# Kernel tuning notes

Measured on AMD Instinct MI355X. Metric: run time of the kernel, lower is better.

## Reference

```python
import jax, jax.numpy as jnp
import numpy as np

N = 32000      # total nodes (16 graphs x 2000 nodes)
B = 16         # batch of graphs
NPG = N // B   # nodes per graph
K = 1600       # assign_dim (total clusters)
KPG = K // B   # clusters per graph
D = 128        # input_dim == output_feat_dim
E = 512000     # edges (avg degree 16), block-diagonal across graphs


def setup_inputs() -> dict:
    key = jax.random.key(0)
    ks = jax.random.split(key, 12)
    # block-structured edge list: each edge stays within its graph
    epg = E // B
    gid = jnp.repeat(jnp.arange(B, dtype=jnp.int32), epg) * NPG
    src = gid + jax.random.randint(ks[0], (E,), 0, NPG, dtype=jnp.int32)
    dst = gid + jax.random.randint(ks[1], (E,), 0, NPG, dtype=jnp.int32)
    h = jax.random.normal(ks[2], (N, D), dtype=jnp.float32)
    s = 0.05
    return {
        'h': h, 'src': src, 'dst': dst,
        'W1f': jax.random.normal(ks[3], (D, D), jnp.float32) * s,
        'b1f': jnp.zeros((D,), jnp.float32),
        'W2f': jax.random.normal(ks[4], (D, D), jnp.float32) * s,
        'b2f': jnp.zeros((D,), jnp.float32),
        'W1p': jax.random.normal(ks[5], (D, K), jnp.float32) * s,
        'b1p': jnp.zeros((K,), jnp.float32),
        'W2p': jax.random.normal(ks[6], (K, K), jnp.float32) * s,
        'b2p': jnp.zeros((K,), jnp.float32),
    }


def _gin(h, src, dst, W1, b1, W2, b2):
    # mean-aggregate neighbor features, then 2-layer MLP (histocartography GINLayer)
    deg = jax.ops.segment_sum(jnp.ones((src.shape[0],), h.dtype), dst, num_segments=N)
    agg = jax.ops.segment_sum(h[src], dst, num_segments=N)
    agg = agg / jnp.maximum(deg, 1.0)[:, None]
    x = h + agg
    x = jax.nn.relu(x @ W1 + b1)
    x = jax.nn.relu(x @ W2 + b2)
    return x


def _forward(h, src, dst, W1f, b1f, W2f, b2f, W1p, b1p, W2p, b2p):
    feat = _gin(h, src, dst, W1f, b1f, W2f, b2f)            # [N, D]
    assign = _gin(h, src, dst, W1p, b1p, W2p, b2p)          # [N, K]
    # block-diagonal mask: node of graph b can only assign to clusters of graph b
    node_gid = jnp.arange(N, dtype=jnp.int32) // NPG
    col_gid = jnp.arange(K, dtype=jnp.int32) // KPG
    mask = (node_gid[:, None] == col_gid[None, :]).astype(assign.dtype)  # [N, K]
    # masked_softmax(memory_efficient=False): softmax(x*mask)*mask, renormalized
    p = jax.nn.softmax(assign * mask, axis=-1) * mask
    assign = p / (jnp.sum(p, axis=-1, keepdims=True) + 1e-13)
    h_pool = assign.T @ feat                                # [K, D]
    # adj @ assign where adj[dst, src] = 1 (sparse-dense mm via scatter)
    tmp = jax.ops.segment_sum(assign[src], dst, num_segments=N)  # [N, K]
    adj_new = assign.T @ tmp                                # [K, K]
    return adj_new, h_pool


def reference(h, src, dst, W1f, b1f, W2f, b2f, W1p, b1p, W2p, b2p):
    return _forward(h, src, dst, W1f, b1f, W2f, b2f, W1p, b1p, W2p, b2p)
```

## Files before the change

kernel.cpp:

```cpp
#include <hip/hip_runtime.h>

#define N_NODES 32000
#define NPG     2000
#define NGRAPH  16
#define K_ASSIGN 1600
#define KPG     100
#define D_FEAT  128
#define N_EDGES 512000

typedef float f32x4 __attribute__((ext_vector_type(4)));
typedef __bf16 bf16x8 __attribute__((ext_vector_type(8)));

union FragU { unsigned u[4]; bf16x8 v; };

__device__ __forceinline__ float frelu(float v) { return fmaxf(v, 0.0f); }

__device__ __forceinline__ unsigned short f2bf(float f) {
  unsigned u = __float_as_uint(f);
  u += 0x7FFFu + ((u >> 16) & 1u);
  return (unsigned short)(u >> 16);
}
__device__ __forceinline__ float bfLO(unsigned v) { return __uint_as_float(v << 16); }
__device__ __forceinline__ float bfHI(unsigned v) { return __uint_as_float(v & 0xFFFF0000u); }

__global__ __launch_bounds__(256) void scan_counts(
    const int* __restrict__ cnt, int* __restrict__ rowstart) {
  __shared__ int sums[256];
  int t = threadIdx.x;
  int base = t * 125;
  int s = 0;
  for (int i = 0; i < 125; i++) s += cnt[base + i];
  sums[t] = s;
  __syncthreads();
  for (int off = 1; off < 256; off <<= 1) {
    int v = (t >= off) ? sums[t - off] : 0;
    __syncthreads();
    sums[t] += v;
    __syncthreads();
  }
  int run = (t == 0) ? 0 : sums[t - 1];
  for (int i = 0; i < 125; i++) {
    rowstart[base + i] = run;
    run += cnt[base + i];
  }
  if (t == 255) rowstart[32000] = run;
}

__global__ __launch_bounds__(256) void edge_fill(
    const int* __restrict__ src, const int* __restrict__ dst,
    const int* __restrict__ rowstart, int* __restrict__ cursor,
    int* __restrict__ bucket) {
  int e = blockIdx.x * 256 + threadIdx.x;
  if (e < N_EDGES) {
    int d = dst[e];
    int pos = atomicAdd(&cursor[d], 1);
    bucket[rowstart[d] + pos] = src[e];
  }
}

__global__ __launch_bounds__(256) void prep_all(
    const float* __restrict__ W1f, const float* __restrict__ W2f,
    const float* __restrict__ W1p, const float* __restrict__ W2p,
    unsigned short* __restrict__ o1, unsigned short* __restrict__ o2,
    unsigned short* __restrict__ o3, unsigned short* __restrict__ o4,
    const float* __restrict__ h, unsigned short* __restrict__ h_bf,
    const int* __restrict__ dst, int* __restrict__ cnt) {
  __shared__ float tile[32][33];
  int b = blockIdx.x;
  int t = threadIdx.x;
  if (b >= 6732) {
    int e = (b - 6732) * 256 + t;
    if (e < N_EDGES) atomicAdd(&cnt[dst[e]], 1);
    return;
  }
  if (b >= 2732) {
    int i = (b - 2732) * 256 + t;
    float4 v = ((const float4*)h)[i];
    ushort4 o;
    o.x = f2bf(v.x); o.y = f2bf(v.y); o.z = f2bf(v.z); o.w = f2bf(v.w);
    ((ushort4*)h_bf)[i] = o;
    return;
  }
  const float* in;
  unsigned short* out;
  int R, C, rb;
  if (b < 16)       { in = W1f; out = o1; R = 128;  C = 128;  rb = b; }
  else if (b < 32)  { in = W2f; out = o2; R = 128;  C = 128;  rb = b - 16; }
  else if (b < 232) { in = W1p; out = o3; R = 128;  C = 1600; rb = b - 32; }
  else              { in = W2p; out = o4; R = 1600; C = 1600; rb = b - 232; }
  int ct = C >> 5;
  int bc = rb % ct, br = rb / ct;
  int r0 = br * 32, c0 = bc * 32;
#pragma unroll
  for (int i = 0; i < 4; i++) {
    int r = (t >> 5) + i * 8, c = t & 31;
    tile[r][c] = in[(size_t)(r0 + r) * C + c0 + c];
  }
  __syncthreads();
#pragma unroll
  for (int i = 0; i < 4; i++) {
    int c = (t >> 5) + i * 8, r = t & 31;
    out[(size_t)(c0 + c) * R + r0 + r] = f2bf(tile[r][c]);
  }
}

__global__ __launch_bounds__(256) void gin_gather(
    const int* __restrict__ rowstart, const int* __restrict__ bucket,
    const unsigned short* __restrict__ h_bf, unsigned short* __restrict__ x_bf) {
  int bid = (int)(blockIdx.x & 7) * 1000 + (int)(blockIdx.x >> 3);
  int n = bid * 4 + (threadIdx.x >> 6);
  int lane = threadIdx.x & 63;
  int rs = rowstart[n], re = rowstart[n + 1];
  const unsigned* hb = (const unsigned*)h_bf;
  float ax = 0.f, ay = 0.f;
  int e = rs;
  for (; e + 4 <= re; e += 4) {
    unsigned v0 = hb[(size_t)bucket[e] * 64 + lane];
    unsigned v1 = hb[(size_t)bucket[e + 1] * 64 + lane];
    unsigned v2 = hb[(size_t)bucket[e + 2] * 64 + lane];
    unsigned v3 = hb[(size_t)bucket[e + 3] * 64 + lane];
    ax += (bfLO(v0) + bfLO(v1)) + (bfLO(v2) + bfLO(v3));
    ay += (bfHI(v0) + bfHI(v1)) + (bfHI(v2) + bfHI(v3));
  }
  for (; e < re; e++) {
    unsigned v = hb[(size_t)bucket[e] * 64 + lane];
    ax += bfLO(v);
    ay += bfHI(v);
  }
  float invd = 1.0f / fmaxf((float)(re - rs), 1.0f);
  unsigned hv = hb[(size_t)n * 64 + lane];
  unsigned o = ((unsigned)f2bf(bfHI(hv) + ay * invd) << 16) |
               f2bf(bfLO(hv) + ax * invd);
  ((unsigned*)x_bf)[(size_t)n * 64 + lane] = o;
}

#define FF_STR 136
__global__ __launch_bounds__(512) void feat_fused(
    const unsigned short* __restrict__ x_bf,
    const unsigned short* __restrict__ w1t, const float* __restrict__ b1f,
    const unsigned short* __restrict__ w2t, const float* __restrict__ b2f,
    unsigned short* __restrict__ feat_bf) {
  __shared__ __align__(16) unsigned char smem[2 * 34816];
  unsigned short* xa = (unsigned short*)smem;
  unsigned short* ws = (unsigned short*)(smem + 34816);
  int t = threadIdx.x;
  size_t base = (size_t)blockIdx.x * 128;

#pragma unroll
  for (int i = 0; i < 4; i++) {
    int fi = t + 512 * i;
    int r = fi >> 4, u8 = (fi & 15) * 8;
    *(uint4*)&xa[r * FF_STR + u8] = *(const uint4*)(x_bf + (base + r) * 128 + u8);
    *(uint4*)&ws[r * FF_STR + u8] = *(const uint4*)(w1t + (size_t)r * 128 + u8);
  }
  __syncthreads();

  int w = t >> 6, l = t & 63, lr = l & 15, lg = l >> 4;
  int myrow = 16 * w + lr;
  bf16x8 af[4];
#pragma unroll
  for (int kc = 0; kc < 4; kc++)
    af[kc] = *(bf16x8*)&xa[myrow * FF_STR + 32 * kc + 8 * lg];

  f32x4 p[8];
#pragma unroll
  for (int ntk = 0; ntk < 8; ntk++) {
    p[ntk] = (f32x4){0.f, 0.f, 0.f, 0.f};
    int c = 16 * ntk + lr;
#pragma unroll
    for (int kc = 0; kc < 4; kc++) {
      bf16x8 wf = *(bf16x8*)&ws[c * FF_STR + 32 * kc + 8 * lg];
      p[ntk] = __builtin_amdgcn_mfma_f32_16x16x32_bf16(wf, af[kc], p[ntk], 0, 0, 0);
    }
  }
  __syncthreads();

#pragma unroll
  for (int ntk = 0; ntk < 8; ntk++) {
    int kk0 = 16 * ntk + 4 * lg;
    float4 b1 = *(const float4*)(b1f + kk0);
    ushort4 pk;
    pk.x = f2bf(frelu(p[ntk][0] + b1.x));
    pk.y = f2bf(frelu(p[ntk][1] + b1.y));
    pk.z = f2bf(frelu(p[ntk][2] + b1.z));
    pk.w = f2bf(frelu(p[ntk][3] + b1.w));
    *(ushort4*)&xa[myrow * FF_STR + kk0] = pk;
  }
#pragma unroll
  for (int i = 0; i < 4; i++) {
    int fi = t + 512 * i;
    int r = fi >> 4, u8 = (fi & 15) * 8;
    *(uint4*)&ws[r * FF_STR + u8] = *(const uint4*)(w2t + (size_t)r * 128 + u8);
  }
  __syncthreads();

  bf16x8 a2[4];
#pragma unroll
  for (int kc = 0; kc < 4; kc++)
    a2[kc] = *(bf16x8*)&xa[myrow * FF_STR + 32 * kc + 8 * lg];
#pragma unroll
  for (int nt = 0; nt < 8; nt++) {
    f32x4 q = (f32x4){0.f, 0.f, 0.f, 0.f};
    int c = 16 * nt + lr;
#pragma unroll
    for (int kc = 0; kc < 4; kc++) {
      bf16x8 wf = *(bf16x8*)&ws[c * FF_STR + 32 * kc + 8 * lg];
      q = __builtin_amdgcn_mfma_f32_16x16x32_bf16(wf, a2[kc], q, 0, 0, 0);
    }
    int c0 = 16 * nt + 4 * lg;
    float4 b2 = *(const float4*)(b2f + c0);
    ushort4 pk;
    pk.x = f2bf(frelu(q[0] + b2.x));
    pk.y = f2bf(frelu(q[1] + b2.y));
    pk.z = f2bf(frelu(q[2] + b2.z));
    pk.w = f2bf(frelu(q[3] + b2.w));
    *(ushort4*)&feat_bf[(base + myrow) * 128 + c0] = pk;
  }
}

#define FA_WS 136
#define FA_PS 72
#define FA_W1OFF 17408
#define FA_W2BASE 34816
#define FA_W2OFF 16128
__global__ __launch_bounds__(512) void fused_assign_sm(
    const unsigned short* __restrict__ x_bf, const unsigned short* __restrict__ w1t,
    const float* __restrict__ b1p, const unsigned short* __restrict__ w2t,
    const float* __restrict__ b2p, unsigned short* __restrict__ assign_bf) {
  __shared__ __align__(16) unsigned char smem[67072];
  unsigned short* xt = (unsigned short*)smem;

  int t = threadIdx.x;
  int g = blockIdx.x >> 4;
  int row0 = (blockIdx.x & 15) << 7;
  int n0 = g * NPG + row0;

#pragma unroll
  for (int i = 0; i < 4; i++) {
    int fi = t + 512 * i;
    int r = fi >> 4, u8 = (fi & 15) * 8;
    uint4 v = make_uint4(0, 0, 0, 0);
    if (row0 + r < NPG) v = *(const uint4*)(x_bf + (size_t)(n0 + r) * 128 + u8);
    *(uint4*)&xt[r * FA_WS + u8] = v;
  }
  __syncthreads();

  int w = t >> 6, l = t & 63, lr = l & 15, lg = l >> 4;
  int rh = w >> 1, h = w & 1;

  bf16x8 af[2][4];
#pragma unroll
  for (int ct = 0; ct < 2; ct++)
#pragma unroll
    for (int kc = 0; kc < 4; kc++)
      af[ct][kc] =
          *(bf16x8*)&xt[(32 * rh + 16 * ct + lr) * FA_WS + 32 * kc + 8 * lg];
  __syncthreads();

  {
    unsigned short* w1s = (unsigned short*)smem;
    unsigned short* w2s = (unsigned short*)(smem + FA_W2BASE);
#pragma unroll
    for (int i = 0; i < 2; i++) {
      int fi = t + 512 * i;
      int c = fi >> 4, u8 = (fi & 15) * 8;
      *(uint4*)&w1s[c * FA_WS + u8] = *(const uint4*)(w1t + (size_t)c * 128 + u8);
    }
#pragma unroll
    for (int i = 0; i < 2; i++) {
      int fi = t + 512 * i;
      if (fi < 896) {
        int c = fi >> 3, u8 = (fi & 7) * 8;
        uint4 v = make_uint4(0, 0, 0, 0);
        if (c < KPG)
          v = *(const uint4*)(w2t + (size_t)(g * KPG + c) * K_ASSIGN + u8);
        *(uint4*)&w2s[c * FA_PS + u8] = v;
      }
    }
  }
  __syncthreads();

  f32x4 acc[7][2];
#pragma unroll
  for (int i = 0; i < 7; i++) {
    acc[i][0] = (f32x4){0.f, 0.f, 0.f, 0.f};
    acc[i][1] = (f32x4){0.f, 0.f, 0.f, 0.f};
  }

  for (int cch = 0; cch < 25; cch++) {
    int cur = cch & 1;
    int k0 = cch * 64;
    const unsigned short* w1c = (const unsigned short*)(smem + cur * FA_W1OFF);
    const unsigned short* w2c =
        (const unsigned short*)(smem + FA_W2BASE + cur * FA_W2OFF);
    bool pf = (cch < 24);
    uint4 rA[2], rB[2];
    if (pf) {
      int k1 = k0 + 64;
#pragma unroll
      for (int i = 0; i < 2; i++) {
        int fi = t + 512 * i;
        int c = fi >> 4, u8 = (fi & 15) * 8;
        rA[i] = *(const uint4*)(w1t + (size_t)(k1 + c) * 128 + u8);
      }
#pragma unroll
      for (int i = 0; i < 2; i++) {
        int fi = t + 512 * i;
        rB[i] = make_uint4(0, 0, 0, 0);
        if (fi < 896) {
          int c = fi >> 3, u8 = (fi & 7) * 8;
          if (c < KPG)
            rB[i] = *(const uint4*)(w2t + (size_t)(g * KPG + c) * K_ASSIGN +
                                    k1 + u8);
        }
      }
    }

    f32x4 p[2][2];
    __builtin_amdgcn_s_setprio(1);
#pragma unroll
    for (int nt2 = 0; nt2 < 2; nt2++) {
      p[nt2][0] = (f32x4){0.f, 0.f, 0.f, 0.f};
      p[nt2][1] = (f32x4){0.f, 0.f, 0.f, 0.f};
      int nt = 2 * h + nt2;
#pragma unroll
      for (int kc = 0; kc < 4; kc++) {
        bf16x8 wf = *(bf16x8*)&w1c[(16 * nt + lr) * FA_WS + 32 * kc + 8 * lg];
        p[nt2][0] = __builtin_amdgcn_mfma_f32_16x16x32_bf16(wf, af[0][kc],
                                                            p[nt2][0], 0, 0, 0);
        p[nt2][1] = __builtin_amdgcn_mfma_f32_16x16x32_bf16(wf, af[1][kc],
                                                            p[nt2][1], 0, 0, 0);
      }
    }
    __builtin_amdgcn_s_setprio(0);
    unsigned q[2][2][2];
#pragma unroll
    for (int nt2 = 0; nt2 < 2; nt2++) {
      int kkb = k0 + 16 * (2 * h + nt2) + 4 * lg;
      float4 b1 = *(const float4*)(b1p + kkb);
#pragma unroll
      for (int ct = 0; ct < 2; ct++) {
        float r0 = frelu(p[nt2][ct][0] + b1.x);
        float r1 = frelu(p[nt2][ct][1] + b1.y);
        float r2 = frelu(p[nt2][ct][2] + b1.z);
        float r3 = frelu(p[nt2][ct][3] + b1.w);
        q[nt2][ct][0] = ((unsigned)f2bf(r1) << 16) | f2bf(r0);
        q[nt2][ct][1] = ((unsigned)f2bf(r3) << 16) | f2bf(r2);
      }
    }
    int sA = lr + 32 * (lg & 1);
    int sB = sA + 16;
    bool hi = (lg >= 2);
    FragU pa[2];
#pragma unroll
    for (int ct = 0; ct < 2; ct++) {
      unsigned a0 = (unsigned)__shfl((int)q[0][ct][0], sA, 64);
      unsigned b0 = (unsigned)__shfl((int)q[1][ct][0], sA, 64);
      unsigned a1 = (unsigned)__shfl((int)q[0][ct][1], sA, 64);
      unsigned b1u = (unsigned)__shfl((int)q[1][ct][1], sA, 64);
      unsigned a2 = (unsigned)__shfl((int)q[0][ct][0], sB, 64);
      unsigned b2u = (unsigned)__shfl((int)q[1][ct][0], sB, 64);
      unsigned a3 = (unsigned)__shfl((int)q[0][ct][1], sB, 64);
      unsigned b3u = (unsigned)__shfl((int)q[1][ct][1], sB, 64);
      pa[ct].u[0] = hi ? b0 : a0;
      pa[ct].u[1] = hi ? b1u : a1;
      pa[ct].u[2] = hi ? b2u : a2;
      pa[ct].u[3] = hi ? b3u : a3;
    }
    __builtin_amdgcn_s_setprio(1);
#pragma unroll
    for (int ct2 = 0; ct2 < 7; ct2++) {
      bf16x8 wv = *(bf16x8*)&w2c[(16 * ct2 + lr) * FA_PS + 32 * h + 8 * lg];
      acc[ct2][0] = __builtin_amdgcn_mfma_f32_16x16x32_bf16(wv, pa[0].v,
                                                            acc[ct2][0], 0, 0, 0);
      acc[ct2][1] = __builtin_amdgcn_mfma_f32_16x16x32_bf16(wv, pa[1].v,
                                                            acc[ct2][1], 0, 0, 0);
    }
    __builtin_amdgcn_s_setprio(0);
    if (pf) {
      unsigned short* w1n = (unsigned short*)(smem + (cur ^ 1) * FA_W1OFF);
      unsigned short* w2n =
          (unsigned short*)(smem + FA_W2BASE + (cur ^ 1) * FA_W2OFF);
#pragma unroll
      for (int i = 0; i < 2; i++) {
        int fi = t + 512 * i;
        int c = fi >> 4, u8 = (fi & 15) * 8;
        *(uint4*)&w1n[c * FA_WS + u8] = rA[i];
      }
#pragma unroll
      for (int i = 0; i < 2; i++) {
        int fi = t + 512 * i;
        if (fi < 896) {
          int c = fi >> 3, u8 = (fi & 7) * 8;
          *(uint4*)&w2n[c * FA_PS + u8] = rB[i];
        }
      }
    }
    __syncthreads();
  }

  float* red = (float*)smem;
  if (h == 1) {
#pragma unroll
    for (int ct2 = 0; ct2 < 7; ct2++)
#pragma unroll
      for (int ct = 0; ct < 2; ct++)
        *(f32x4*)&red[((rh * 14 + ct2 * 2 + ct) * 64 + l) * 4] = acc[ct2][ct];
  }
  __syncthreads();
  if (h == 0) {
#pragma unroll
    for (int ct2 = 0; ct2 < 7; ct2++)
#pragma unroll
      for (int ct = 0; ct < 2; ct++)
        acc[ct2][ct] += *(f32x4*)&red[((rh * 14 + ct2 * 2 + ct) * 64 + l) * 4];

#pragma unroll
    for (int ct = 0; ct < 2; ct++) {
      int xrow = row0 + 32 * rh + 16 * ct + lr;
      float v[7][4];
      float m = 0.0f;
#pragma unroll
      for (int ct2 = 0; ct2 < 7; ct2++) {
        int col0 = 16 * ct2 + 4 * lg;
        if (col0 < KPG) {
          float4 b2 = *(const float4*)(b2p + g * KPG + col0);
          v[ct2][0] = frelu(acc[ct2][ct][0] + b2.x);
          v[ct2][1] = frelu(acc[ct2][ct][1] + b2.y);
          v[ct2][2] = frelu(acc[ct2][ct][2] + b2.z);
          v[ct2][3] = frelu(acc[ct2][ct][3] + b2.w);
          m = fmaxf(m, fmaxf(fmaxf(v[ct2][0], v[ct2][1]),
                             fmaxf(v[ct2][2], v[ct2][3])));
        }
      }
      m = fmaxf(m, __shfl_xor(m, 16, 64));
      m = fmaxf(m, __shfl_xor(m, 32, 64));
      float s = 0.0f;
#pragma unroll
      for (int ct2 = 0; ct2 < 7; ct2++) {
        int col0 = 16 * ct2 + 4 * lg;
        if (col0 < KPG) {
          v[ct2][0] = expf(v[ct2][0] - m);
          v[ct2][1] = expf(v[ct2][1] - m);
          v[ct2][2] = expf(v[ct2][2] - m);
          v[ct2][3] = expf(v[ct2][3] - m);
          s += (v[ct2][0] + v[ct2][1]) + (v[ct2][2] + v[ct2][3]);
        }
      }
      s += __shfl_xor(s, 16, 64);
      s += __shfl_xor(s, 32, 64);
      float denom = s + (float)(K_ASSIGN - KPG) * expf(-m);
      float scale = 1.0f / (s + 1e-13f * denom);
      if (xrow < NPG) {
#pragma unroll
        for (int ct2 = 0; ct2 < 7; ct2++) {
          int col0 = 16 * ct2 + 4 * lg;
          if (col0 < KPG) {
            ushort4 pk;
            pk.x = f2bf(v[ct2][0] * scale);
            pk.y = f2bf(v[ct2][1] * scale);
            pk.z = f2bf(v[ct2][2] * scale);
            pk.w = f2bf(v[ct2][3] * scale);
            *(ushort4*)(assign_bf + ((size_t)g * NPG + xrow) * KPG + col0) = pk;
          }
        }
      }
    }
  }
}

__global__ __launch_bounds__(256) void tmp_gather(
    const int* __restrict__ rowstart, const int* __restrict__ bucket,
    const unsigned short* __restrict__ assign_bf, unsigned short* __restrict__ tmp_bf) {
  int bid = (int)(blockIdx.x & 7) * 1000 + (int)(blockIdx.x >> 3);
  int n = bid * 4 + (threadIdx.x >> 6);
  int lane = threadIdx.x & 63;
  if (lane >= 50) return;
  int rs = rowstart[n], re = rowstart[n + 1];
  const unsigned* ab = (const unsigned*)assign_bf;
  float ax = 0.f, ay = 0.f;
  int e = rs;
  for (; e + 4 <= re; e += 4) {
    unsigned v0 = ab[(size_t)bucket[e] * 50 + lane];
    unsigned v1 = ab[(size_t)bucket[e + 1] * 50 + lane];
    unsigned v2 = ab[(size_t)bucket[e + 2] * 50 + lane];
    unsigned v3 = ab[(size_t)bucket[e + 3] * 50 + lane];
    ax += (bfLO(v0) + bfLO(v1)) + (bfLO(v2) + bfLO(v3));
    ay += (bfHI(v0) + bfHI(v1)) + (bfHI(v2) + bfHI(v3));
  }
  for (; e < re; e++) {
    unsigned v = ab[(size_t)bucket[e] * 50 + lane];
    ax += bfLO(v);
    ay += bfHI(v);
  }
  unsigned o = ((unsigned)f2bf(ay) << 16) | f2bf(ax);
  ((unsigned*)tmp_bf)[(size_t)n * 50 + lane] = o;
}

#define PA_STR 72
#define PA_CH 16
#define PA_CHN 128
__global__ __launch_bounds__(256) void pool_adj_mfma(
    const unsigned short* __restrict__ assign_bf,
    const unsigned short* __restrict__ feat_bf,
    const unsigned short* __restrict__ tmp_bf,
    float* __restrict__ out_adj, float* __restrict__ out_hpool) {
  __shared__ __align__(16) unsigned short as[112 * PA_STR];
  __shared__ __align__(16) unsigned short bs[128 * PA_STR];
  bool is_pool = blockIdx.x < NGRAPH * PA_CH;
  int bb = is_pool ? blockIdx.x : blockIdx.x - NGRAPH * PA_CH;
  int g = bb >> 4, ch = bb & 15;
  int nbase = ch * PA_CHN;
  int lim = NPG - nbase;
  if (lim > PA_CHN) lim = PA_CHN;
  int t = threadIdx.x;
  int w = t >> 6, l = t & 63, lr = l & 15, lg = l >> 4;
  const unsigned* au = (const unsigned*)assign_bf;
  const unsigned* fu = (const unsigned*)feat_bf;
  const unsigned* tu = (const unsigned*)tmp_bf;

  for (int i = t; i < 12 * PA_STR; i += 256) as[100 * PA_STR + i] = 0;
  for (int i = t; i < 28 * PA_STR; i += 256) bs[100 * PA_STR + i] = 0;

  f32x4 acc[7][2];
#pragma unroll
  for (int i = 0; i < 7; i++) {
    acc[i][0] = (f32x4){0.f, 0.f, 0.f, 0.f};
    acc[i][1] = (f32x4){0.f, 0.f, 0.f, 0.f};
  }

  for (int kt = 0; kt < 2; kt++) {
    int nt0 = kt * 64;
    __syncthreads();
#pragma unroll
    for (int i = 0; i < 13; i++) {
      int idx = t + 256 * i;
      if (idx < 3200) {
        int r = idx / 50, cu = idx % 50;
        int nl = nt0 + r;
        unsigned v = 0;
        if (nl < lim) v = au[(size_t)(g * NPG + nbase + nl) * 50 + cu];
        as[(2 * cu) * PA_STR + r] = (unsigned short)(v & 0xFFFFu);
        as[(2 * cu + 1) * PA_STR + r] = (unsigned short)(v >> 16);
      }
    }
    if (is_pool) {
#pragma unroll
      for (int i = 0; i < 16; i++) {
        int idx = t + 256 * i;
        int r = idx >> 6, cu = idx & 63;
        int nl = nt0 + r;
        unsigned v = 0;
        if (nl < lim) v = fu[(size_t)(g * NPG + nbase + nl) * 64 + cu];
        bs[(2 * cu) * PA_STR + r] = (unsigned short)(v & 0xFFFFu);
        bs[(2 * cu + 1) * PA_STR + r] = (unsigned short)(v >> 16);
      }
    } else {
#pragma unroll
      for (int i = 0; i < 13; i++) {
        int idx = t + 256 * i;
        if (idx < 3200) {
          int r = idx / 50, cu = idx % 50;
          int nl = nt0 + r;
          unsigned v = 0;
          if (nl < lim) v = tu[(size_t)(g * NPG + nbase + nl) * 50 + cu];
          bs[(2 * cu) * PA_STR + r] = (unsigned short)(v & 0xFFFFu);
          bs[(2 * cu + 1) * PA_STR + r] = (unsigned short)(v >> 16);
        }
      }
    }
    __syncthreads();
#pragma unroll
    for (int kc = 0; kc < 2; kc++) {
      bf16x8 afr[7];
#pragma unroll
      for (int mt = 0; mt < 7; mt++)
        afr[mt] = *(bf16x8*)&as[(16 * mt + lr) * PA_STR + 32 * kc + 8 * lg];
#pragma unroll
      for (int nt2 = 0; nt2 < 2; nt2++) {
        int nt = 2 * w + nt2;
        bf16x8 bfr = *(bf16x8*)&bs[(16 * nt + lr) * PA_STR + 32 * kc + 8 * lg];
#pragma unroll
        for (int mt = 0; mt < 7; mt++)
          acc[mt][nt2] =
              __builtin_amdgcn_mfma_f32_16x16x32_bf16(afr[mt], bfr, acc[mt][nt2], 0, 0, 0);
      }
    }
  }

  if (is_pool) {
#pragma unroll
    for (int mt = 0; mt < 7; mt++)
#pragma unroll
      for (int nt2 = 0; nt2 < 2; nt2++) {
        int nt = 2 * w + nt2;
#pragma unroll
        for (int r = 0; r < 4; r++) {
          int m = 16 * mt + 4 * lg + r;
          if (m < KPG)
            atomicAdd(out_hpool + ((size_t)g * KPG + m) * 128 + 16 * nt + lr,
                      acc[mt][nt2][r]);
        }
      }
  } else {
#pragma unroll
    for (int mt = 0; mt < 7; mt++)
#pragma unroll
      for (int nt2 = 0; nt2 < 2; nt2++) {
        int nt = 2 * w + nt2;
        if (nt < 7) {
          int k2 = 16 * nt + lr;
          if (k2 < KPG) {
#pragma unroll
            for (int r = 0; r < 4; r++) {
              int m = 16 * mt + 4 * lg + r;
              if (m < KPG)
                atomicAdd(out_adj + ((size_t)g * KPG + m) * K_ASSIGN + g * KPG + k2,
                          acc[mt][nt2][r]);
            }
          }
        }
      }
  }
}

extern "C" void kernel_launch(void* const* d_in, const int* in_sizes, int n_in,
                              void* d_out, int out_size, void* d_ws,
                              size_t ws_size, hipStream_t stream) {
  (void)in_sizes; (void)n_in; (void)ws_size;
  const float* h   = (const float*)d_in[0];
  const int*   src = (const int*)d_in[1];
  const int*   dst = (const int*)d_in[2];
  const float* W1f = (const float*)d_in[3];
  const float* b1f = (const float*)d_in[4];
  const float* W2f = (const float*)d_in[5];
  const float* b2f = (const float*)d_in[6];
  const float* W1p = (const float*)d_in[7];
  const float* b1p = (const float*)d_in[8];
  const float* W2p = (const float*)d_in[9];
  const float* b2p = (const float*)d_in[10];

  float* out_adj   = (float*)d_out;
  float* out_hpool = out_adj + (size_t)K_ASSIGN * K_ASSIGN;

  char* ws = (char*)d_ws;
  int* deg_cnt  = (int*)(ws + 0);
  int* rowstart = (int*)(ws + 128000);
  int* cursor   = (int*)(ws + 256032);
  int* bucket   = (int*)(ws + 384032);
  unsigned short* h_bf      = (unsigned short*)(ws + 2432032);
  unsigned short* x_bf      = (unsigned short*)(ws + 10624032);
  unsigned short* feat_bf   = (unsigned short*)(ws + 18816032);
  unsigned short* assign_bf = (unsigned short*)(ws + 27008032);
  unsigned short* tmp_bf    = (unsigned short*)(ws + 33408032);
  unsigned short* w1f_t     = (unsigned short*)(ws + 39808032);
  unsigned short* w2f_t     = (unsigned short*)(ws + 39840800);
  unsigned short* w1p_t     = (unsigned short*)(ws + 39873568);
  unsigned short* w2p_t     = (unsigned short*)(ws + 40283168);

  hipMemsetAsync(deg_cnt, 0, 128000, stream);
  hipMemsetAsync(cursor, 0, 128000, stream);
  hipMemsetAsync(d_out, 0, (size_t)out_size * sizeof(float), stream);

  prep_all<<<8732, 256, 0, stream>>>(W1f, W2f, W1p, W2p, w1f_t, w2f_t, w1p_t,
                                     w2p_t, h, h_bf, dst, deg_cnt);

  scan_counts<<<1, 256, 0, stream>>>(deg_cnt, rowstart);
  edge_fill<<<N_EDGES / 256, 256, 0, stream>>>(src, dst, rowstart, cursor, bucket);

  gin_gather<<<N_NODES / 4, 256, 0, stream>>>(rowstart, bucket, h_bf, x_bf);

  feat_fused<<<N_NODES / 128, 512, 0, stream>>>(x_bf, w1f_t, b1f, w2f_t, b2f, feat_bf);

  fused_assign_sm<<<256, 512, 0, stream>>>(x_bf, w1p_t, b1p, w2p_t, b2p, assign_bf);

  tmp_gather<<<N_NODES / 4, 256, 0, stream>>>(rowstart, bucket, assign_bf, tmp_bf);

  pool_adj_mfma<<<NGRAPH * PA_CH * 2, 256, 0, stream>>>(
      assign_bf, feat_bf, tmp_bf, out_adj, out_hpool);
}
```

Measured before the change: 228.3 us.

## Merge independent kernels into shared launches and widen scan to 1024 threads

Merges the feature MLP and the assignment MLP into one launch, with block index choosing the branch, so the two independent GEMM stages can run concurrently. Also folds the pooled-feature GEMM into the adjacency gather launch, leaving a separate adjacency GEMM kernel that depends on tmp. The single-block prefix scan now uses 1024 threads, each handling 32 counts instead of 125. This is meant to cut launch count and tail idle time, but the merged kernels carry the larger shared-memory footprint on every block, which may lower occupancy for the lighter branches.

After: 246.4 us. +7.9%, slower.

```diff
diff --git a/kernel.cpp b/kernel.cpp
--- a/kernel.cpp
+++ b/kernel.cpp
@@ -22,41 +22,6 @@
 }
 __device__ __forceinline__ float bfLO(unsigned v) { return __uint_as_float(v << 16); }
 __device__ __forceinline__ float bfHI(unsigned v) { return __uint_as_float(v & 0xFFFF0000u); }
-
-__global__ __launch_bounds__(256) void scan_counts(
-    const int* __restrict__ cnt, int* __restrict__ rowstart) {
-  __shared__ int sums[256];
-  int t = threadIdx.x;
-  int base = t * 125;
-  int s = 0;
-  for (int i = 0; i < 125; i++) s += cnt[base + i];
-  sums[t] = s;
-  __syncthreads();
-  for (int off = 1; off < 256; off <<= 1) {
-    int v = (t >= off) ? sums[t - off] : 0;
-    __syncthreads();
-    sums[t] += v;
-    __syncthreads();
-  }
-  int run = (t == 0) ? 0 : sums[t - 1];
-  for (int i = 0; i < 125; i++) {
-    rowstart[base + i] = run;
-    run += cnt[base + i];
-  }
-  if (t == 255) rowstart[32000] = run;
-}
-
-__global__ __launch_bounds__(256) void edge_fill(
-    const int* __restrict__ src, const int* __restrict__ dst,
-    const int* __restrict__ rowstart, int* __restrict__ cursor,
-    int* __restrict__ bucket) {
-  int e = blockIdx.x * 256 + threadIdx.x;
-  if (e < N_EDGES) {
-    int d = dst[e];
-    int pos = atomicAdd(&cursor[d], 1);
-    bucket[rowstart[d] + pos] = src[e];
-  }
-}
 
 __global__ __launch_bounds__(256) void prep_all(
     const float* __restrict__ W1f, const float* __restrict__ W2f,
@@ -101,6 +66,44 @@
   for (int i = 0; i < 4; i++) {
     int c = (t >> 5) + i * 8, r = t & 31;
     out[(size_t)(c0 + c) * R + r0 + r] = f2bf(tile[r][c]);
+  }
+}
+
+__global__ __launch_bounds__(1024) void scan_counts(
+    const int* __restrict__ cnt, int* __restrict__ rowstart) {
+  __shared__ int sums[1024];
+  int t = threadIdx.x;
+  int base = t * 32;
+  int s = 0;
+  if (t < 1000)
+    for (int i = 0; i < 32; i++) s += cnt[base + i];
+  sums[t] = s;
+  __syncthreads();
+  for (int off = 1; off < 1024; off <<= 1) {
+    int v = (t >= off) ? sums[t - off] : 0;
+    __syncthreads();
+    sums[t] += v;
+    __syncthreads();
+  }
+  if (t < 1000) {
+    int run = (t == 0) ? 0 : sums[t - 1];
+    for (int i = 0; i < 32; i++) {
+      rowstart[base + i] = run;
+      run += cnt[base + i];
+    }
+  }
+  if (t == 999) rowstart[32000] = sums[999];
+}
+
+__global__ __launch_bounds__(256) void edge_fill(
+    const int* __restrict__ src, const int* __restrict__ dst,
+    const int* __restrict__ rowstart, int* __restrict__ cursor,
+    int* __restrict__ bucket) {
+  int e = blockIdx.x * 256 + threadIdx.x;
+  if (e < N_EDGES) {
+    int d = dst[e];
+    int pos = atomicAdd(&cursor[d], 1);
+    bucket[rowstart[d] + pos] = src[e];
   }
 }
 
@@ -135,102 +138,101 @@
 }
 
 #define FF_STR 136
-__global__ __launch_bounds__(512) void feat_fused(
-    const unsigned short* __restrict__ x_bf,
-    const unsigned short* __restrict__ w1t, const float* __restrict__ b1f,
-    const unsigned short* __restrict__ w2t, const float* __restrict__ b2f,
-    unsigned short* __restrict__ feat_bf) {
-  __shared__ __align__(16) unsigned char smem[2 * 34816];
-  unsigned short* xa = (unsigned short*)smem;
-  unsigned short* ws = (unsigned short*)(smem + 34816);
-  int t = threadIdx.x;
-  size_t base = (size_t)blockIdx.x * 128;
-
-#pragma unroll
-  for (int i = 0; i < 4; i++) {
-    int fi = t + 512 * i;
-    int r = fi >> 4, u8 = (fi & 15) * 8;
-    *(uint4*)&xa[r * FF_STR + u8] = *(const uint4*)(x_bf + (base + r) * 128 + u8);
-    *(uint4*)&ws[r * FF_STR + u8] = *(const uint4*)(w1t + (size_t)r * 128 + u8);
-  }
-  __syncthreads();
-
-  int w = t >> 6, l = t & 63, lr = l & 15, lg = l >> 4;
-  int myrow = 16 * w + lr;
-  bf16x8 af[4];
-#pragma unroll
-  for (int kc = 0; kc < 4; kc++)
-    af[kc] = *(bf16x8*)&xa[myrow * FF_STR + 32 * kc + 8 * lg];
-
-  f32x4 p[8];
-#pragma unroll
-  for (int ntk = 0; ntk < 8; ntk++) {
-    p[ntk] = (f32x4){0.f, 0.f, 0.f, 0.f};
-    int c = 16 * ntk + lr;
-#pragma unroll
-    for (int kc = 0; kc < 4; kc++) {
-      bf16x8 wf = *(bf16x8*)&ws[c * FF_STR + 32 * kc + 8 * lg];
-      p[ntk] = __builtin_amdgcn_mfma_f32_16x16x32_bf16(wf, af[kc], p[ntk], 0, 0, 0);
-    }
-  }
-  __syncthreads();
-
-#pragma unroll
-  for (int ntk = 0; ntk < 8; ntk++) {
-    int kk0 = 16 * ntk + 4 * lg;
-    float4 b1 = *(const float4*)(b1f + kk0);
-    ushort4 pk;
-    pk.x = f2bf(frelu(p[ntk][0] + b1.x));
-    pk.y = f2bf(frelu(p[ntk][1] + b1.y));
-    pk.z = f2bf(frelu(p[ntk][2] + b1.z));
-    pk.w = f2bf(frelu(p[ntk][3] + b1.w));
-    *(ushort4*)&xa[myrow * FF_STR + kk0] = pk;
-  }
-#pragma unroll
-  for (int i = 0; i < 4; i++) {
-    int fi = t + 512 * i;
-    int r = fi >> 4, u8 = (fi & 15) * 8;
-    *(uint4*)&ws[r * FF_STR + u8] = *(const uint4*)(w2t + (size_t)r * 128 + u8);
-  }
-  __syncthreads();
-
-  bf16x8 a2[4];
-#pragma unroll
-  for (int kc = 0; kc < 4; kc++)
-    a2[kc] = *(bf16x8*)&xa[myrow * FF_STR + 32 * kc + 8 * lg];
-#pragma unroll
-  for (int nt = 0; nt < 8; nt++) {
-    f32x4 q = (f32x4){0.f, 0.f, 0.f, 0.f};
-    int c = 16 * nt + lr;
-#pragma unroll
-    for (int kc = 0; kc < 4; kc++) {
-      bf16x8 wf = *(bf16x8*)&ws[c * FF_STR + 32 * kc + 8 * lg];
-      q = __builtin_amdgcn_mfma_f32_16x16x32_bf16(wf, a2[kc], q, 0, 0, 0);
-    }
-    int c0 = 16 * nt + 4 * lg;
-    float4 b2 = *(const float4*)(b2f + c0);
-    ushort4 pk;
-    pk.x = f2bf(frelu(q[0] + b2.x));
-    pk.y = f2bf(frelu(q[1] + b2.y));
-    pk.z = f2bf(frelu(q[2] + b2.z));
-    pk.w = f2bf(frelu(q[3] + b2.w));
-    *(ushort4*)&feat_bf[(base + myrow) * 128 + c0] = pk;
-  }
-}
-
 #define FA_WS 136
 #define FA_PS 72
 #define FA_W1OFF 17408
 #define FA_W2BASE 34816
 #define FA_W2OFF 16128
-__global__ __launch_bounds__(512) void fused_assign_sm(
-    const unsigned short* __restrict__ x_bf, const unsigned short* __restrict__ w1t,
-    const float* __restrict__ b1p, const unsigned short* __restrict__ w2t,
-    const float* __restrict__ b2p, unsigned short* __restrict__ assign_bf) {
-  __shared__ __align__(16) unsigned char smem[67072];
+__global__ __launch_bounds__(512) void feat_assign(
+    const unsigned short* __restrict__ x_bf,
+    const unsigned short* __restrict__ w1ft, const float* __restrict__ b1f,
+    const unsigned short* __restrict__ w2ft, const float* __restrict__ b2f,
+    unsigned short* __restrict__ feat_bf,
+    const unsigned short* __restrict__ w1t, const float* __restrict__ b1p,
+    const unsigned short* __restrict__ w2t, const float* __restrict__ b2p,
+    unsigned short* __restrict__ assign_bf) {
+  __shared__ __align__(16) unsigned char smem[69632];
+  int t = threadIdx.x;
+  int w = t >> 6, l = t & 63, lr = l & 15, lg = l >> 4;
+
+  if (blockIdx.x >= 256) {
+    unsigned short* xa = (unsigned short*)smem;
+    unsigned short* ws = (unsigned short*)(smem + 34816);
+    size_t base = (size_t)(blockIdx.x - 256) * 128;
+
+#pragma unroll
+    for (int i = 0; i < 4; i++) {
+      int fi = t + 512 * i;
+      int r = fi >> 4, u8 = (fi & 15) * 8;
+      *(uint4*)&xa[r * FF_STR + u8] = *(const uint4*)(x_bf + (base + r) * 128 + u8);
+      *(uint4*)&ws[r * FF_STR + u8] = *(const uint4*)(w1ft + (size_t)r * 128 + u8);
+    }
+    __syncthreads();
+
+    int myrow = 16 * w + lr;
+    bf16x8 af[4];
+#pragma unroll
+    for (int kc = 0; kc < 4; kc++)
+      af[kc] = *(bf16x8*)&xa[myrow * FF_STR + 32 * kc + 8 * lg];
+
+    f32x4 p[8];
+#pragma unroll
+    for (int ntk = 0; ntk < 8; ntk++) {
+      p[ntk] = (f32x4){0.f, 0.f, 0.f, 0.f};
+      int c = 16 * ntk + lr;
+#pragma unroll
+      for (int kc = 0; kc < 4; kc++) {
+        bf16x8 wf = *(bf16x8*)&ws[c * FF_STR + 32 * kc + 8 * lg];
+        p[ntk] = __builtin_amdgcn_mfma_f32_16x16x32_bf16(wf, af[kc], p[ntk], 0, 0, 0);
+      }
+    }
+    __syncthreads();
+
+#pragma unroll
+    for (int ntk = 0; ntk < 8; ntk++) {
+      int kk0 = 16 * ntk + 4 * lg;
+      float4 b1 = *(const float4*)(b1f + kk0);
+      ushort4 pk;
+      pk.x = f2bf(frelu(p[ntk][0] + b1.x));
+      pk.y = f2bf(frelu(p[ntk][1] + b1.y));
+      pk.z = f2bf(frelu(p[ntk][2] + b1.z));
+      pk.w = f2bf(frelu(p[ntk][3] + b1.w));
+      *(ushort4*)&xa[myrow * FF_STR + kk0] = pk;
+    }
+#pragma unroll
+    for (int i = 0; i < 4; i++) {
+      int fi = t + 512 * i;
+      int r = fi >> 4, u8 = (fi & 15) * 8;
+      *(uint4*)&ws[r * FF_STR + u8] = *(const uint4*)(w2ft + (size_t)r * 128 + u8);
+    }
+    __syncthreads();
+
+    bf16x8 a2[4];
+#pragma unroll
+    for (int kc = 0; kc < 4; kc++)
+      a2[kc] = *(bf16x8*)&xa[myrow * FF_STR + 32 * kc + 8 * lg];
+#pragma unroll
+    for (int nt = 0; nt < 8; nt++) {
+      f32x4 q = (f32x4){0.f, 0.f, 0.f, 0.f};
+      int c = 16 * nt + lr;
+#pragma unroll
+      for (int kc = 0; kc < 4; kc++) {
+        bf16x8 wf = *(bf16x8*)&ws[c * FF_STR + 32 * kc + 8 * lg];
+        q = __builtin_amdgcn_mfma_f32_16x16x32_bf16(wf, a2[kc], q, 0, 0, 0);
+      }
+      int c0 = 16 * nt + 4 * lg;
+      float4 b2 = *(const float4*)(b2f + c0);
+      ushort4 pk;
+      pk.x = f2bf(frelu(q[0] + b2.x));
+      pk.y = f2bf(frelu(q[1] + b2.y));
+      pk.z = f2bf(frelu(q[2] + b2.z));
+      pk.w = f2bf(frelu(q[3] + b2.w));
+      *(ushort4*)&feat_bf[(base + myrow) * 128 + c0] = pk;
+    }
+    return;
+  }
+
   unsigned short* xt = (unsigned short*)smem;
-
-  int t = threadIdx.x;
   int g = blockIdx.x >> 4;
   int row0 = (blockIdx.x & 15) << 7;
   int n0 = g * NPG + row0;
@@ -245,7 +247,6 @@
   }
   __syncthreads();
 
-  int w = t >> 6, l = t & 63, lr = l & 15, lg = l >> 4;
   int rh = w >> 1, h = w & 1;
 
   bf16x8 af[2][4];
@@ -469,58 +470,54 @@
   }
 }
 
-__global__ __launch_bounds__(256) void tmp_gather(
+#define PA_STR 72
+#define PA_CHN 128
+__global__ __launch_bounds__(256) void tmp_pool(
     const int* __restrict__ rowstart, const int* __restrict__ bucket,
-    const unsigned short* __restrict__ assign_bf, unsigned short* __restrict__ tmp_bf) {
-  int bid = (int)(blockIdx.x & 7) * 1000 + (int)(blockIdx.x >> 3);
-  int n = bid * 4 + (threadIdx.x >> 6);
-  int lane = threadIdx.x & 63;
-  if (lane >= 50) return;
-  int rs = rowstart[n], re = rowstart[n + 1];
-  const unsigned* ab = (const unsigned*)assign_bf;
-  float ax = 0.f, ay = 0.f;
-  int e = rs;
-  for (; e + 4 <= re; e += 4) {
-    unsigned v0 = ab[(size_t)bucket[e] * 50 + lane];
-    unsigned v1 = ab[(size_t)bucket[e + 1] * 50 + lane];
-    unsigned v2 = ab[(size_t)bucket[e + 2] * 50 + lane];
-    unsigned v3 = ab[(size_t)bucket[e + 3] * 50 + lane];
-    ax += (bfLO(v0) + bfLO(v1)) + (bfLO(v2) + bfLO(v3));
-    ay += (bfHI(v0) + bfHI(v1)) + (bfHI(v2) + bfHI(v3));
-  }
-  for (; e < re; e++) {
-    unsigned v = ab[(size_t)bucket[e] * 50 + lane];
-    ax += bfLO(v);
-    ay += bfHI(v);
-  }
-  unsigned o = ((unsigned)f2bf(ay) << 16) | f2bf(ax);
-  ((unsigned*)tmp_bf)[(size_t)n * 50 + lane] = o;
-}
-
-#define PA_STR 72
-#define PA_CH 16
-#define PA_CHN 128
-__global__ __launch_bounds__(256) void pool_adj_mfma(
     const unsigned short* __restrict__ assign_bf,
     const unsigned short* __restrict__ feat_bf,
-    const unsigned short* __restrict__ tmp_bf,
-    float* __restrict__ out_adj, float* __restrict__ out_hpool) {
+    unsigned short* __restrict__ tmp_bf, float* __restrict__ out_hpool) {
   __shared__ __align__(16) unsigned short as[112 * PA_STR];
   __shared__ __align__(16) unsigned short bs[128 * PA_STR];
-  bool is_pool = blockIdx.x < NGRAPH * PA_CH;
-  int bb = is_pool ? blockIdx.x : blockIdx.x - NGRAPH * PA_CH;
+  int t = threadIdx.x;
+
+  if (blockIdx.x < 8000) {
+    int bid = (int)(blockIdx.x & 7) * 1000 + (int)(blockIdx.x >> 3);
+    int n = bid * 4 + (t >> 6);
+    int lane = t & 63;
+    if (lane >= 50) return;
+    int rs = rowstart[n], re = rowstart[n + 1];
+    const unsigned* ab = (const unsigned*)assign_bf;
+    float ax = 0.f, ay = 0.f;
+    int e = rs;
+    for (; e + 4 <= re; e += 4) {
+      unsigned v0 = ab[(size_t)bucket[e] * 50 + lane];
+      unsigned v1 = ab[(size_t)bucket[e + 1] * 50 + lane];
+      unsigned v2 = ab[(size_t)bucket[e + 2] * 50 + lane];
+      unsigned v3 = ab[(size_t)bucket[e + 3] * 50 + lane];
+      ax += (bfLO(v0) + bfLO(v1)) + (bfLO(v2) + bfLO(v3));
+      ay += (bfHI(v0) + bfHI(v1)) + (bfHI(v2) + bfHI(v3));
+    }
+    for (; e < re; e++) {
+      unsigned v = ab[(size_t)bucket[e] * 50 + lane];
+      ax += bfLO(v);
+      ay += bfHI(v);
+    }
+    unsigned o = ((unsigned)f2bf(ay) << 16) | f2bf(ax);
+    ((unsigned*)tmp_bf)[(size_t)n * 50 + lane] = o;
+    return;
+  }
+
+  int bb = blockIdx.x - 8000;
   int g = bb >> 4, ch = bb & 15;
   int nbase = ch * PA_CHN;
   int lim = NPG - nbase;
   if (lim > PA_CHN) lim = PA_CHN;
-  int t = threadIdx.x;
   int w = t >> 6, l = t & 63, lr = l & 15, lg = l >> 4;
   const unsigned* au = (const unsigned*)assign_bf;
   const unsigned* fu = (const unsigned*)feat_bf;
-  const unsigned* tu = (const unsigned*)tmp_bf;
 
   for (int i = t; i < 12 * PA_STR; i += 256) as[100 * PA_STR + i] = 0;
-  for (int i = t; i < 28 * PA_STR; i += 256) bs[100 * PA_STR + i] = 0;
 
   f32x4 acc[7][2];
 #pragma unroll
@@ -544,30 +541,15 @@
         as[(2 * cu + 1) * PA_STR + r] = (unsigned short)(v >> 16);
       }
     }
-    if (is_pool) {
-#pragma unroll
-      for (int i = 0; i < 16; i++) {
-        int idx = t + 256 * i;
-        int r = idx >> 6, cu = idx & 63;
-        int nl = nt0 + r;
-        unsigned v = 0;
-        if (nl < lim) v = fu[(size_t)(g * NPG + nbase + nl) * 64 + cu];
-        bs[(2 * cu) * PA_STR + r] = (unsigned short)(v & 0xFFFFu);
-        bs[(2 * cu + 1) * PA_STR + r] = (unsigned short)(v >> 16);
-      }
-    } else {
-#pragma unroll
-      for (int i = 0; i < 13; i++) {
-        int idx = t + 256 * i;
-        if (idx < 3200) {
-          int r = idx / 50, cu = idx % 50;
-          int nl = nt0 + r;
-          unsigned v = 0;
-          if (nl < lim) v = tu[(size_t)(g * NPG + nbase + nl) * 50 + cu];
-          bs[(2 * cu) * PA_STR + r] = (unsigned short)(v & 0xFFFFu);
-          bs[(2 * cu + 1) * PA_STR + r] = (unsigned short)(v >> 16);
-        }
-      }
+#pragma unroll
+    for (int i = 0; i < 16; i++) {
+      int idx = t + 256 * i;
+      int r = idx >> 6, cu = idx & 63;
+      int nl = nt0 + r;
+      unsigned v = 0;
+      if (nl < lim) v = fu[(size_t)(g * NPG + nbase + nl) * 64 + cu];
+      bs[(2 * cu) * PA_STR + r] = (unsigned short)(v & 0xFFFFu);
+      bs[(2 * cu + 1) * PA_STR + r] = (unsigned short)(v >> 16);
     }
     __syncthreads();
 #pragma unroll
@@ -588,40 +570,103 @@
     }
   }
 
-  if (is_pool) {
-#pragma unroll
-    for (int mt = 0; mt < 7; mt++)
+#pragma unroll
+  for (int mt = 0; mt < 7; mt++)
+#pragma unroll
+    for (int nt2 = 0; nt2 < 2; nt2++) {
+      int nt = 2 * w + nt2;
+#pragma unroll
+      for (int r = 0; r < 4; r++) {
+        int m = 16 * mt + 4 * lg + r;
+        if (m < KPG)
+          atomicAdd(out_hpool + ((size_t)g * KPG + m) * 128 + 16 * nt + lr,
+                    acc[mt][nt2][r]);
+      }
+    }
+}
+
+__global__ __launch_bounds__(256) void adj_mfma(
+    const unsigned short* __restrict__ assign_bf,
+    const unsigned short* __restrict__ tmp_bf, float* __restrict__ out_adj) {
+  __shared__ __align__(16) unsigned short as[112 * PA_STR];
+  __shared__ __align__(16) unsigned short bs[128 * PA_STR];
+  int bb = blockIdx.x;
+  int g = bb >> 4, ch = bb & 15;
+  int nbase = ch * PA_CHN;
+  int lim = NPG - nbase;
+  if (lim > PA_CHN) lim = PA_CHN;
+  int t = threadIdx.x;
+  int w = t >> 6, l = t & 63, lr = l & 15, lg = l >> 4;
+  const unsigned* au = (const unsigned*)assign_bf;
+  const unsigned* tu = (const unsigned*)tmp_bf;
+
+  for (int i = t; i < 12 * PA_STR; i += 256) as[100 * PA_STR + i] = 0;
+  for (int i = t; i < 28 * PA_STR; i += 256) bs[100 * PA_STR + i] = 0;
+
+  f32x4 acc[7][2];
+#pragma unroll
+  for (int i = 0; i < 7; i++) {
+    acc[i][0] = (f32x4){0.f, 0.f, 0.f, 0.f};
+    acc[i][1] = (f32x4){0.f, 0.f, 0.f, 0.f};
+  }
+
+  for (int kt = 0; kt < 2; kt++) {
+    int nt0 = kt * 64;
+    __syncthreads();
+#pragma unroll
+    for (int i = 0; i < 13; i++) {
+      int idx = t + 256 * i;
+      if (idx < 3200) {
+        int r = idx / 50, cu = idx % 50;
+        int nl = nt0 + r;
+        unsigned v = 0, v2 = 0;
+        if (nl < lim) {
+          v = au[(size_t)(g * NPG + nbase + nl) * 50 + cu];
+          v2 = tu[(size_t)(g * NPG + nbase + nl) * 50 + cu];
+        }
+        as[(2 * cu) * PA_STR + r] = (unsigned short)(v & 0xFFFFu);
+        as[(2 * cu + 1) * PA_STR + r] = (unsigned short)(v >> 16);
+        bs[(2 * cu) * PA_STR + r] = (unsigned short)(v2 & 0xFFFFu);
+        bs[(2 * cu + 1) * PA_STR + r] = (unsigned short)(v2 >> 16);
+      }
+    }
+    __syncthreads();
+#pragma unroll
+    for (int kc = 0; kc < 2; kc++) {
+      bf16x8 afr[7];
+#pragma unroll
+      for (int mt = 0; mt < 7; mt++)
+        afr[mt] = *(bf16x8*)&as[(16 * mt + lr) * PA_STR + 32 * kc + 8 * lg];
 #pragma unroll
       for (int nt2 = 0; nt2 < 2; nt2++) {
         int nt = 2 * w + nt2;
-#pragma unroll
-        for (int r = 0; r < 4; r++) {
-          int m = 16 * mt + 4 * lg + r;
-          if (m < KPG)
-            atomicAdd(out_hpool + ((size_t)g * KPG + m) * 128 + 16 * nt + lr,
-                      acc[mt][nt2][r]);
-        }
-      }
-  } else {
-#pragma unroll
-    for (int mt = 0; mt < 7; mt++)
-#pragma unroll
-      for (int nt2 = 0; nt2 < 2; nt2++) {
-        int nt = 2 * w + nt2;
-        if (nt < 7) {
-          int k2 = 16 * nt + lr;
-          if (k2 < KPG) {
-#pragma unroll
-            for (int r = 0; r < 4; r++) {
-              int m = 16 * mt + 4 * lg + r;
-              if (m < KPG)
-                atomicAdd(out_adj + ((size_t)g * KPG + m) * K_ASSIGN + g * KPG + k2,
-                          acc[mt][nt2][r]);
-            }
+        bf16x8 bfr = *(bf16x8*)&bs[(16 * nt + lr) * PA_STR + 32 * kc + 8 * lg];
+#pragma unroll
+        for (int mt = 0; mt < 7; mt++)
+          acc[mt][nt2] =
+              __builtin_amdgcn_mfma_f32_16x16x32_bf16(afr[mt], bfr, acc[mt][nt2], 0, 0, 0);
+      }
+    }
+  }
+
+#pragma unroll
+  for (int mt = 0; mt < 7; mt++)
+#pragma unroll
+    for (int nt2 = 0; nt2 < 2; nt2++) {
+      int nt = 2 * w + nt2;
+      if (nt < 7) {
+        int k2 = 16 * nt + lr;
+        if (k2 < KPG) {
+#pragma unroll
+          for (int r = 0; r < 4; r++) {
+            int m = 16 * mt + 4 * lg + r;
+            if (m < KPG)
+              atomicAdd(out_adj + ((size_t)g * KPG + m) * K_ASSIGN + g * KPG + k2,
+                        acc[mt][nt2][r]);
           }
         }
       }
-  }
+    }
 }
 
 extern "C" void kernel_launch(void* const* d_in, const int* in_sizes, int n_in,
@@ -665,17 +710,17 @@
   prep_all<<<8732, 256, 0, stream>>>(W1f, W2f, W1p, W2p, w1f_t, w2f_t, w1p_t,
                                      w2p_t, h, h_bf, dst, deg_cnt);
 
-  scan_counts<<<1, 256, 0, stream>>>(deg_cnt, rowstart);
+  scan_counts<<<1, 1024, 0, stream>>>(deg_cnt, rowstart);
   edge_fill<<<N_EDGES / 256, 256, 0, stream>>>(src, dst, rowstart, cursor, bucket);
 
   gin_gather<<<N_NODES / 4, 256, 0, stream>>>(rowstart, bucket, h_bf, x_bf);
 
-  feat_fused<<<N_NODES / 128, 512, 0, stream>>>(x_bf, w1f_t, b1f, w2f_t, b2f, feat_bf);
-
-  fused_assign_sm<<<256, 512, 0, stream>>>(x_bf, w1p_t, b1p, w2p_t, b2p, assign_bf);
-
-  tmp_gather<<<N_NODES / 4, 256, 0, stream>>>(rowstart, bucket, assign_bf, tmp_bf);
-
-  pool_adj_mfma<<<NGRAPH * PA_CH * 2, 256, 0, stream>>>(
-      assign_bf, feat_bf, tmp_bf, out_adj, out_hpool);
-}
+  feat_assign<<<256 + N_NODES / 128, 512, 0, stream>>>(
+      x_bf, w1f_t, b1f, w2f_t, b2f, feat_bf,
+      w1p_t, b1p, w2p_t, b2p, assign_bf);
+
+  tmp_pool<<<8000 + 256, 256, 0, stream>>>(rowstart, bucket, assign_bf,
+                                           feat_bf, tmp_bf, out_hpool);
+
+  adj_mfma<<<256, 256, 0, stream>>>(assign_bf, tmp_bf, out_adj);
+}
```
